# Performance work log

Measured on AMD Instinct MI355X. Metric: run time of the kernel, lower is better.

Reference implementation:

```python
import jax, jax.numpy as jnp
import numpy as np

N_NODES, N_EDGES, B, L = 20000, 320000, 64, 48
EMB, OUT, HEADS, HID = 256, 64, 4, 512
S_DIM, R_DIM = 64, 64
TIME_NUM, CAT_NUM = 48, 201


def lrelu(x, s=0.2):
    return jnp.where(x >= 0, x, s * x)


def gru_cell(x, h, Wi, Wh, bi, bh):
    # PyTorch GRUCell math
    gi = x @ Wi.T + bi
    gh = h @ Wh.T + bh
    ir, iz, ig = jnp.split(gi, 3, axis=-1)
    hr, hz, hg = jnp.split(gh, 3, axis=-1)
    r = jax.nn.sigmoid(ir + hr)
    z = jax.nn.sigmoid(iz + hz)
    n = jnp.tanh(ig + r * hg)
    return (1.0 - z) * n + z * h


def gru_seq(x, Wi, Wh, bi, bh, reverse=False):
    # x: [B,L,D] -> [B,L,H]
    xs = jnp.swapaxes(x, 0, 1)
    if reverse:
        xs = xs[::-1]
    h0 = jnp.zeros((x.shape[0], Wh.shape[1]), x.dtype)

    def step(h, xt):
        h2 = gru_cell(xt, h, Wi, Wh, bi, bh)
        return h2, h2

    _, ys = jax.lax.scan(step, h0, xs)
    if reverse:
        ys = ys[::-1]
    return jnp.swapaxes(ys, 0, 1)


def setup_inputs() -> dict:
    key = jax.random.key(0)
    ks = iter(jax.random.split(key, 64))
    f32 = jnp.float32

    def rn(shape, s=0.1):
        return (s * jax.random.normal(next(ks), shape)).astype(f32)

    inp = {
        'graph_x': jnp.arange(N_NODES),
        'edge_index': jax.random.randint(next(ks), (2, N_EDGES), 0, N_NODES),
        'edge_attr': jax.random.uniform(next(ks), (N_EDGES,), f32),
        'batch_x': jax.random.randint(next(ks), (B, L), 0, N_NODES),
        'batch_time': jax.random.randint(next(ks), (B, L), 0, TIME_NUM),
        'batch_cat': jax.random.randint(next(ks), (B, L), 0, CAT_NUM),
        'poi_time': jax.random.randint(next(ks), (N_NODES,), 0, TIME_NUM),
        'poi_cat': jax.random.randint(next(ks), (N_NODES,), 0, CAT_NUM),
        # params
        'node_emb': rn((N_NODES, EMB), 1.0),
        'W_gat': rn((EMB, HEADS * OUT), 0.05),
        'att_src': rn((HEADS, OUT), 0.05),
        'att_dst': rn((HEADS, OUT), 0.05),
        'gat_bias': rn((HEADS * OUT,)),
        'time_table': rn((TIME_NUM, EMB), 1.0),
        'cat_table': rn((CAT_NUM, EMB), 1.0),
        'W_w': rn((EMB, 3 * EMB)), 'b_w': rn((EMB,)),
        'Wi_f': rn((3 * HID, EMB), 0.05), 'Wh_f': rn((3 * HID, HID), 0.05),
        'bi_f': jnp.zeros((3 * HID,), f32), 'bh_f': jnp.zeros((3 * HID,), f32),
        'Wi_bw': rn((3 * HID, EMB), 0.05), 'Wh_bw': rn((3 * HID, HID), 0.05),
        'bi_bw': jnp.zeros((3 * HID,), f32), 'bh_bw': jnp.zeros((3 * HID,), f32),
        'Wi_u': rn((3 * HID, 2 * HID), 0.05), 'Wh_u': rn((3 * HID, HID), 0.05),
        'bi_u': jnp.zeros((3 * HID,), f32), 'bh_u': jnp.zeros((3 * HID,), f32),
        'Ws_m': rn((S_DIM, 2 * HID)), 'bs_m': rn((S_DIM,)),
        'Ws_lv': rn((S_DIM, 2 * HID)), 'bs_lv': rn((S_DIM,)),
        'Wr_m': rn((R_DIM, HID)), 'br_m': rn((R_DIM,)),
        'Wr_lv': rn((R_DIM, HID)), 'br_lv': rn((R_DIM,)),
        'Wp1_i': rn((3 * HID, R_DIM), 0.05), 'Wp1_h': rn((3 * HID, HID), 0.05),
        'bp1_i': jnp.zeros((3 * HID,), f32), 'bp1_h': jnp.zeros((3 * HID,), f32),
        'Wp2_i': rn((3 * HID, HID), 0.05), 'Wp2_h': rn((3 * HID, HID), 0.05),
        'bp2_i': jnp.zeros((3 * HID,), f32), 'bp2_h': jnp.zeros((3 * HID,), f32),
        'Wpm': rn((R_DIM, HID)), 'bpm': rn((R_DIM,)),
        'Wplv': rn((R_DIM, HID)), 'bplv': rn((R_DIM,)),
        'Wd': rn((N_NODES, S_DIM + R_DIM)), 'bd': rn((N_NODES,)),
    }
    return inp


def forward(graph_x, edge_index, edge_attr, batch_x, batch_time, batch_cat,
            poi_time, poi_cat, node_emb, W_gat, att_src, att_dst, gat_bias,
            time_table, cat_table, W_w, b_w, Wi_f, Wh_f, bi_f, bh_f,
            Wi_bw, Wh_bw, bi_bw, bh_bw, Wi_u, Wh_u, bi_u, bh_u,
            Ws_m, bs_m, Ws_lv, bs_lv, Wr_m, br_m, Wr_lv, br_lv,
            Wp1_i, Wp1_h, bp1_i, bp1_h, Wp2_i, Wp2_h, bp2_i, bp2_h,
            Wpm, bpm, Wplv, bplv, Wd, bd):
    Bn, Ln = batch_x.shape
    N = node_emb.shape[0]
    heads, C = att_src.shape

    # --- weighted GAT layer over the POI graph ---
    h = node_emb[graph_x]                                   # [N, EMB]
    xW = (h @ W_gat).reshape(N, heads, C)                   # [N, H, C]
    src, dst = edge_index[0], edge_index[1]
    e = lrelu((xW * att_src).sum(-1)[src] + (xW * att_dst).sum(-1)[dst])  # [E, H]
    emax = jax.ops.segment_max(e, dst, num_segments=N)
    a = jnp.exp(e - emax[dst])
    asum = jax.ops.segment_sum(a, dst, num_segments=N)
    att = a / (asum[dst] + 1e-16)
    msg = (att * edge_attr[:, None])[:, :, None] * xW[src]  # [E, H, C]
    p = jax.ops.segment_sum(msg, dst, num_segments=N).reshape(N, heads * C) + gat_bias

    # --- per-step feature build ---
    p_h = p[batch_x]                                        # [B, L, EMB]
    t_e = time_table[batch_time]
    c_e = cat_table[batch_cat]
    ph = jnp.concatenate([p_h, t_e, c_e], axis=2) @ W_w.T + b_w  # [B, L, EMB]

    # --- posterior encode: biGRU -> s, uniGRU -> r ---
    f_fwd = gru_seq(ph, Wi_f, Wh_f, bi_f, bh_f)
    f_bwd = gru_seq(ph, Wi_bw, Wh_bw, bi_bw, bh_bw, reverse=True)
    features = jnp.concatenate([f_fwd, f_bwd], axis=2)      # [B, L, 2H]
    Hh = Wh_f.shape[1]
    frontal = features[:, Ln - 1, :Hh]
    backward = features[:, 0, Hh:2 * Hh]
    g = jnp.concatenate([frontal, backward], axis=1)
    s_mean = lrelu(g @ Ws_m.T + bs_m)
    s_logvar = lrelu(g @ Ws_lv.T + bs_lv)

    key = jax.random.key(42)
    k1, k2, k3 = jax.random.split(key, 3)
    s_post = s_mean + jax.random.normal(k1, s_mean.shape, s_mean.dtype) * jnp.exp(0.5 * s_logvar)

    r_feat = gru_seq(features, Wi_u, Wh_u, bi_u, bh_u)      # [B, L, H]
    r_mean = r_feat @ Wr_m.T + br_m
    r_logvar = r_feat @ Wr_lv.T + br_lv
    r_post = r_mean + jax.random.normal(k2, r_mean.shape, r_mean.dtype) * jnp.exp(0.5 * r_logvar)

    # --- prior: 2-layer GRUCell unroll fed with shifted r_post ---
    Rd = r_post.shape[2]
    r_in = jnp.concatenate([jnp.zeros((Bn, 1, Rd), r_post.dtype), r_post[:, :-1]], axis=1)
    r_in_t = jnp.swapaxes(r_in, 0, 1)                       # [L, B, R]
    eps = jax.random.normal(k3, (Ln, Bn, Rd), r_post.dtype)

    def pstep(carry, xe):
        h1, h2 = carry
        rt, ep = xe
        h1 = gru_cell(rt, h1, Wp1_i, Wp1_h, bp1_i, bp1_h)
        h2 = gru_cell(h1, h2, Wp2_i, Wp2_h, bp2_i, bp2_h)
        mt = h2 @ Wpm.T + bpm
        lvt = h2 @ Wplv.T + bplv
        rp = mt + ep * jnp.exp(0.5 * lvt)
        return (h1, h2), (mt, lvt, rp)

    h10 = jnp.zeros((Bn, Hh), r_post.dtype)
    h20 = jnp.zeros((Bn, Hh), r_post.dtype)
    _, (ms, lvs, rps) = jax.lax.scan(pstep, (h10, h20), (r_in_t, eps))
    r_mean_prior = jnp.swapaxes(ms, 0, 1)
    r_logvar_prior = jnp.swapaxes(lvs, 0, 1)
    r_prior = jnp.swapaxes(rps, 0, 1)

    # --- decode ---
    s_expand = jnp.broadcast_to(s_post[:, None, :], (Bn, Ln, s_post.shape[1]))
    zf = jnp.concatenate([r_post, s_expand], axis=2)
    recon_x = zf @ Wd.T + bd                                # [B, L, node_num]
    return (s_mean, s_logvar, s_post, r_mean, r_logvar, r_post,
            r_mean_prior, r_logvar_prior, r_prior, recon_x)


def reference(graph_x, edge_index, edge_attr, batch_x, batch_time, batch_cat,
              poi_time, poi_cat, node_emb, W_gat, att_src, att_dst, gat_bias,
              time_table, cat_table, W_w, b_w, Wi_f, Wh_f, bi_f, bh_f,
              Wi_bw, Wh_bw, bi_bw, bh_bw, Wi_u, Wh_u, bi_u, bh_u,
              Ws_m, bs_m, Ws_lv, bs_lv, Wr_m, br_m, Wr_lv, br_lv,
              Wp1_i, Wp1_h, bp1_i, bp1_h, Wp2_i, Wp2_h, bp2_i, bp2_h,
              Wpm, bpm, Wplv, bplv, Wd, bd):
    return forward(graph_x, edge_index, edge_attr, batch_x, batch_time, batch_cat,
                   poi_time, poi_cat, node_emb, W_gat, att_src, att_dst, gat_bias,
                   time_table, cat_table, W_w, b_w, Wi_f, Wh_f, bi_f, bh_f,
                   Wi_bw, Wh_bw, bi_bw, bh_bw, Wi_u, Wh_u, bi_u, bh_u,
                   Ws_m, bs_m, Ws_lv, bs_lv, Wr_m, br_m, Wr_lv, br_lv,
                   Wp1_i, Wp1_h, bp1_i, bp1_h, Wp2_i, Wp2_h, bp2_i, bp2_h,
                   Wpm, bpm, Wplv, bplv, Wd, bd)
```

## Files before the change

kernel.cpp:

```cpp
#include <hip/hip_runtime.h>
#include <stdint.h>
#include <stddef.h>

#define DEV __device__ __forceinline__

typedef float f32x4 __attribute__((ext_vector_type(4)));
typedef short bf16x8 __attribute__((ext_vector_type(8)));

__host__ __device__ inline void tf2x32(uint32_t k0, uint32_t k1,
                                       uint32_t x0, uint32_t x1,
                                       uint32_t* o0, uint32_t* o1) {
  uint32_t ks2 = k0 ^ k1 ^ 0x1BD11BDAu;
  uint32_t ks[3] = {k0, k1, ks2};
  x0 += k0; x1 += k1;
  const uint32_t R[8] = {13u,15u,26u,6u,17u,29u,16u,24u};
  for (int r = 0; r < 5; ++r) {
    const uint32_t* rot = (r & 1) ? (R + 4) : R;
    for (int i = 0; i < 4; ++i) {
      x0 += x1;
      uint32_t d = rot[i];
      x1 = (x1 << d) | (x1 >> (32u - d));
      x1 ^= x0;
    }
    x0 += ks[(r + 1) % 3];
    x1 += ks[(r + 2) % 3] + (uint32_t)(r + 1);
  }
  *o0 = x0; *o1 = x1;
}

DEV float erfinv_approx(float x) {
  float w = -logf((1.0f - x) * (1.0f + x));
  float p;
  if (w < 5.0f) {
    w = w - 2.5f;
    p = 2.81022636e-08f;
    p = fmaf(p, w, 3.43273939e-07f);
    p = fmaf(p, w, -3.5233877e-06f);
    p = fmaf(p, w, -4.39150654e-06f);
    p = fmaf(p, w, 0.00021858087f);
    p = fmaf(p, w, -0.00125372503f);
    p = fmaf(p, w, -0.00417768164f);
    p = fmaf(p, w, 0.246640727f);
    p = fmaf(p, w, 1.50140941f);
  } else {
    w = sqrtf(w) - 3.0f;
    p = -0.000200214257f;
    p = fmaf(p, w, 0.000100950558f);
    p = fmaf(p, w, 0.00134934322f);
    p = fmaf(p, w, -0.00367342844f);
    p = fmaf(p, w, 0.00573950773f);
    p = fmaf(p, w, -0.0076224613f);
    p = fmaf(p, w, 0.00943887047f);
    p = fmaf(p, w, 1.00167406f);
    p = fmaf(p, w, 2.83297682f);
  }
  return p * x;
}

DEV float normal_part(uint32_t ka, uint32_t kb, uint32_t idx) {
  uint32_t b1, b2;
  tf2x32(ka, kb, 0u, idx, &b1, &b2);
  uint32_t bits = b1 ^ b2;
  float f = __uint_as_float((bits >> 9) | 0x3f800000u) - 1.0f;
  const float lo = -0.99999994f;
  float u = f * 2.0f + lo;
  u = fmaxf(lo, u);
  return 1.41421356f * erfinv_approx(u);
}

DEV float lrelu(float x) { return x >= 0.f ? x : 0.2f * x; }
DEV float sigm(float x) { return 1.0f / (1.0f + expf(-x)); }

DEV float gru_out(float ir, float iz, float ig, float hr, float hz, float hg, float hprev) {
  float r = sigm(ir + hr);
  float z = sigm(iz + hz);
  float n = tanhf(ig + r * hg);
  return (1.0f - z) * n + z * hprev;
}

DEV float dot4f(float4 a, float4 b, float acc) {
  return fmaf(a.x, b.x, fmaf(a.y, b.y, fmaf(a.z, b.z, fmaf(a.w, b.w, acc))));
}

template <int K4>
DEV void dot2(const float* __restrict__ h, const float* __restrict__ w0,
              const float* __restrict__ w1, float& a0, float& a1) {
  const float4* h4 = (const float4*)h;
  const float4* p0 = (const float4*)w0;
  const float4* p1 = (const float4*)w1;
  #pragma unroll 4
  for (int k = 0; k < K4; ++k) {
    float4 hv = h4[k];
    float4 v0 = p0[k], v1 = p1[k];
    a0 = dot4f(hv, v0, a0);
    a1 = dot4f(hv, v1, a1);
  }
}

template <int K4>
DEV void dotT3p(const float* __restrict__ hp, int b,
                const float* __restrict__ w0, const float* __restrict__ w1,
                const float* __restrict__ w2, float& a0, float& a1, float& a2) {
  const float4* __restrict__ w04 = (const float4*)w0;
  const float4* __restrict__ w14 = (const float4*)w1;
  const float4* __restrict__ w24 = (const float4*)w2;
  const float4* __restrict__ h4 = (const float4*)hp;
  #pragma unroll
  for (int k4 = 0; k4 < K4; ++k4) {
    float4 hv = h4[k4 * 64 + b];
    a0 = dot4f(w04[k4], hv, a0);
    a1 = dot4f(w14[k4], hv, a1);
    a2 = dot4f(w24[k4], hv, a2);
  }
}

template <int K4>
DEV void dotT3_lds(const float* __restrict__ hl, int b,
                   const float* __restrict__ w0, const float* __restrict__ w1,
                   const float* __restrict__ w2, float& a0, float& a1, float& a2) {
  const float4* __restrict__ h4 = (const float4*)hl;
  const float4* __restrict__ w04 = (const float4*)w0;
  const float4* __restrict__ w14 = (const float4*)w1;
  const float4* __restrict__ w24 = (const float4*)w2;
  #pragma unroll 8
  for (int k4 = 0; k4 < K4; ++k4) {
    float4 hv = h4[k4 * 64 + b];
    a0 = dot4f(w04[k4], hv, a0);
    a1 = dot4f(w14[k4], hv, a1);
    a2 = dot4f(w24[k4], hv, a2);
  }
}

template <int N16>
DEV void stage_lds(float* __restrict__ dst, const float* __restrict__ src) {
  const float4* __restrict__ s4 = (const float4*)src;
  float4* __restrict__ d4 = (float4*)dst;
  int tid = threadIdx.x;
  constexpr int CH = (N16 < 16) ? N16 : 16;
  #pragma unroll
  for (int r = 0; r < N16; r += CH) {
    float4 v[CH];
    #pragma unroll
    for (int u = 0; u < CH; ++u) v[u] = s4[(size_t)(r + u) * 256 + tid];
    #pragma unroll
    for (int u = 0; u < CH; ++u) d4[(size_t)(r + u) * 256 + tid] = v[u];
  }
}

DEV size_t pk(int k, int b) { return (size_t)(k >> 2) * 256 + b * 4 + (k & 3); }

DEV void coh_store_i(int* p, int v) {
  asm volatile("global_store_dword %0, %1, off sc0 sc1" :: "v"(p), "v"(v) : "memory");
}
DEV void coh_store_f(float* p, float v) {
  asm volatile("global_store_dword %0, %1, off sc0 sc1" :: "v"(p), "v"(v) : "memory");
}
DEV void coh_store_f4(float* p, f32x4 v) {
  asm volatile("global_store_dwordx4 %0, %1, off sc0 sc1" :: "v"(p), "v"(v) : "memory");
}
DEV int coh_load_i(const int* p) {
  int v;
  asm volatile("global_load_dword %0, %1, off sc0 sc1\n\ts_waitcnt vmcnt(0)"
               : "=v"(v) : "v"(p) : "memory");
  return v;
}

#define FSTRIDE 32

DEV void flag_barrier(int* __restrict__ flags, int nblk, int myidx, int gen) {
  asm volatile("s_waitcnt vmcnt(0)" ::: "memory");
  __syncthreads();
  if (threadIdx.x == 0) coh_store_i(flags + (size_t)myidx * FSTRIDE, gen);
  if ((int)threadIdx.x < nblk) {
    int spins = 0;
    while (coh_load_i(flags + (size_t)threadIdx.x * FSTRIDE) < gen) {
      __builtin_amdgcn_s_sleep(4);
      if (++spins > (1 << 21)) break;
    }
  }
  __syncthreads();
}

DEV void wait_group(const int* __restrict__ flags, int nblk, int thr) {
  if ((int)threadIdx.x < nblk) {
    int spins = 0;
    while (coh_load_i(flags + (size_t)threadIdx.x * FSTRIDE) < thr) {
      __builtin_amdgcn_s_sleep(4);
      if (++spins > (1 << 21)) break;
    }
  }
  __syncthreads();
}

DEV void store_packed_tile4(float* dst_t, const float (*smem)[64], int j0) {
  if (threadIdx.x < 64) {
    int bb = threadIdx.x;
    f32x4 v;
    v.x = smem[0][bb];
    v.y = smem[1][bb];
    v.z = smem[2][bb];
    v.w = smem[3][bb];
    coh_store_f4(dst_t + (size_t)(j0 >> 2) * 256 + bb * 4, v);
  }
}

#define GBM 128
#define GBN 128
#define GBK 16

__global__ __launch_bounds__(256) void gemm_nt(
    const float* __restrict__ A, const float* __restrict__ Bt,
    const float* __restrict__ bias, float* __restrict__ C,
    int M, int N, int K, const int* __restrict__ gatherA, int trGI) {
  __shared__ float As[GBK][GBM + 4];
  __shared__ float Bs[GBK][GBN + 4];
  const int bm = blockIdx.y * GBM;
  const int bn = blockIdx.x * GBN;
  const int tid = threadIdx.x;
  const int tx = tid & 15;
  const int ty = tid >> 4;
  float acc[8][8];
  #pragma unroll
  for (int i = 0; i < 8; ++i)
    #pragma unroll
    for (int j = 0; j < 8; ++j) acc[i][j] = 0.f;

  for (int k0 = 0; k0 < K; k0 += GBK) {
    #pragma unroll
    for (int s = 0; s < 2; ++s) {
      int f = tid + s * 256;
      int r = f >> 2, kq = f & 3;
      int row = bm + r;
      float4 v = make_float4(0.f, 0.f, 0.f, 0.f);
      if (row < M) {
        int ar = gatherA ? gatherA[row] : row;
        v = *(const float4*)&A[(size_t)ar * K + k0 + kq * 4];
      }
      As[kq * 4 + 0][r] = v.x;
      As[kq * 4 + 1][r] = v.y;
      As[kq * 4 + 2][r] = v.z;
      As[kq * 4 + 3][r] = v.w;
    }
    #pragma unroll
    for (int s = 0; s < 2; ++s) {
      int f = tid + s * 256;
      int r = f >> 2, kq = f & 3;
      int col = bn + r;
      float4 v = make_float4(0.f, 0.f, 0.f, 0.f);
      if (col < N) v = *(const float4*)&Bt[(size_t)col * K + k0 + kq * 4];
      Bs[kq * 4 + 0][r] = v.x;
      Bs[kq * 4 + 1][r] = v.y;
      Bs[kq * 4 + 2][r] = v.z;
      Bs[kq * 4 + 3][r] = v.w;
    }
    __syncthreads();
    #pragma unroll
    for (int kk = 0; kk < GBK; ++kk) {
      float4 a0 = *(const float4*)&As[kk][ty * 4];
      float4 a1 = *(const float4*)&As[kk][64 + ty * 4];
      float4 b0 = *(const float4*)&Bs[kk][tx * 4];
      float4 b1 = *(const float4*)&Bs[kk][64 + tx * 4];
      float av[8] = {a0.x, a0.y, a0.z, a0.w, a1.x, a1.y, a1.z, a1.w};
      float bv[8] = {b0.x, b0.y, b0.z, b0.w, b1.x, b1.y, b1.z, b1.w};
      #pragma unroll
      for (int i = 0; i < 8; ++i)
        #pragma unroll
        for (int j = 0; j < 8; ++j)
          acc[i][j] = fmaf(av[i], bv[j], acc[i][j]);
    }
    __syncthreads();
  }
  #pragma unroll
  for (int i = 0; i < 8; ++i) {
    int row = bm + ((i < 4) ? (ty * 4 + i) : (64 + ty * 4 + i - 4));
    if (row >= M) continue;
    if (trGI) {
      #pragma unroll
      for (int j = 0; j < 8; ++j) {
        int col = bn + ((j < 4) ? (tx * 4 + j) : (64 + tx * 4 + j - 4));
        if (col >= N) continue;
        float v = acc[i][j] + (bias ? bias[col] : 0.f);
        int bb = row / 48, tt = row - bb * 48;
        C[((size_t)tt * N + col) * 64 + bb] = v;
      }
    } else {
      #pragma unroll
      for (int g = 0; g < 2; ++g) {
        int col0 = bn + g * 64 + tx * 4;
        if (col0 + 3 >= N) continue;
        float4 v;
        v.x = acc[i][g * 4 + 0] + (bias ? bias[col0 + 0] : 0.f);
        v.y = acc[i][g * 4 + 1] + (bias ? bias[col0 + 1] : 0.f);
        v.z = acc[i][g * 4 + 2] + (bias ? bias[col0 + 2] : 0.f);
        v.w = acc[i][g * 4 + 3] + (bias ? bias[col0 + 3] : 0.f);
        *(float4*)&C[(size_t)row * N + col0] = v;
      }
    }
  }
}

__global__ void k_f32_to_bf16(const float* __restrict__ src,
                              unsigned short* __restrict__ dst, int n) {
  int i = blockIdx.x * 256 + threadIdx.x;
  if (i >= n) return;
  uint32_t u = __float_as_uint(src[i]);
  uint32_t r = (u + 0x7fffu + ((u >> 16) & 1u)) >> 16;
  dst[i] = (unsigned short)r;
}

__global__ __launch_bounds__(256) void gemm_bf16_mfma(
    const unsigned short* __restrict__ A16, const unsigned short* __restrict__ B16,
    const float* __restrict__ bias, float* __restrict__ C,
    int M, int N, int K, int trGI) {
  int bm = blockIdx.x * 128;
  int bn = blockIdx.y * 128;
  int wave = threadIdx.x >> 6;
  int lane = threadIdx.x & 63;
  int wm = (wave & 1) * 64;
  int wn = (wave >> 1) * 64;
  int l15 = lane & 15;
  int kg = lane >> 4;
  f32x4 acc[4][4];
  #pragma unroll
  for (int mi = 0; mi < 4; ++mi)
    #pragma unroll
    for (int ni = 0; ni < 4; ++ni)
      acc[mi][ni] = (f32x4){0.f, 0.f, 0.f, 0.f};

  for (int kk = 0; kk < K; kk += 32) {
    bf16x8 afrag[4], bfrag[4];
    #pragma unroll
    for (int mi = 0; mi < 4; ++mi) {
      int row = bm + wm + mi * 16 + l15;
      afrag[mi] = *(const bf16x8*)&A16[(size_t)row * K + kk + kg * 8];
    }
    #pragma unroll
    for (int ni = 0; ni < 4; ++ni) {
      int col = bn + wn + ni * 16 + l15;
      if (col >= N) col = N - 1;
      bfrag[ni] = *(const bf16x8*)&B16[(size_t)col * K + kk + kg * 8];
    }
    #pragma unroll
    for (int mi = 0; mi < 4; ++mi)
      #pragma unroll
      for (int ni = 0; ni < 4; ++ni)
        acc[mi][ni] = __builtin_amdgcn_mfma_f32_16x16x32_bf16(
            afrag[mi], bfrag[ni], acc[mi][ni], 0, 0, 0);
  }
  #pragma unroll
  for (int mi = 0; mi < 4; ++mi) {
    #pragma unroll
    for (int ni = 0; ni < 4; ++ni) {
      int col = bn + wn + ni * 16 + l15;
      if (col >= N) continue;
      int rowb = bm + wm + mi * 16 + kg * 4;
      float bv = bias ? bias[col] : 0.f;
      if (trGI) {
        #pragma unroll
        for (int r = 0; r < 4; ++r) {
          int row = rowb + r;
          int bb = row / 48, tt = row - bb * 48;
          C[((size_t)tt * N + col) * 64 + bb] = acc[mi][ni][r] + bv;
        }
      } else {
        #pragma unroll
        for (int r = 0; r < 4; ++r)
          C[(size_t)(rowb + r) * N + col] = acc[mi][ni][r] + bv;
      }
    }
  }
}

__global__ void k_transpose(const float* __restrict__ W, float* __restrict__ Wt,
                            int rows, int cols) {
  int idx = blockIdx.x * 256 + threadIdx.x;
  if (idx >= rows * cols) return;
  int r = idx / cols, c = idx % cols;
  Wt[(size_t)c * rows + r] = W[idx];
}

__global__ void k_count_deg(const int* __restrict__ dst, int* __restrict__ deg, int nE) {
  int e = blockIdx.x * 256 + threadIdx.x;
  if (e < nE) atomicAdd(&deg[dst[e]], 1);
}

__global__ __launch_bounds__(1024) void k_scan(const int* __restrict__ deg,
                                               int* __restrict__ off,
                                               int* __restrict__ cursor, int n) {
  __shared__ int tmp[1024];
  __shared__ int carry_s;
  if (threadIdx.x == 0) carry_s = 0;
  __syncthreads();
  for (int base = 0; base < n; base += 1024) {
    int i = base + (int)threadIdx.x;
    int v = (i < n) ? deg[i] : 0;
    tmp[threadIdx.x] = v;
    __syncthreads();
    for (int s = 1; s < 1024; s <<= 1) {
      int t = (threadIdx.x >= (unsigned)s) ? tmp[threadIdx.x - s] : 0;
      __syncthreads();
      tmp[threadIdx.x] += t;
      __syncthreads();
    }
    int incl = tmp[threadIdx.x];
    int base_c = carry_s;
    int excl = incl - v;
    if (i < n) { off[i] = base_c + excl; cursor[i] = base_c + excl; }
    __syncthreads();
    if (threadIdx.x == 1023) carry_s = base_c + incl;
    __syncthreads();
  }
  if (threadIdx.x == 0) off[n] = carry_s;
}

__global__ void k_scatter(const int* __restrict__ dst, int* __restrict__ cursor,
                          int* __restrict__ csr, int nE) {
  int e = blockIdx.x * 256 + threadIdx.x;
  if (e < nE) {
    int pos = atomicAdd(&cursor[dst[e]], 1);
    csr[pos] = e;
  }
}

__global__ void k_alpha(const float* __restrict__ xW, const float* __restrict__ att_src,
                        const float* __restrict__ att_dst, float* __restrict__ as_,
                        float* __restrict__ ad_) {
  int i = blockIdx.x * 256 + threadIdx.x;
  if (i >= 80000) return;
  int n = i >> 2, h = i & 3;
  const float* xr = xW + (size_t)n * 256 + h * 64;
  const float* s = att_src + h * 64;
  const float* d = att_dst + h * 64;
  float a = 0.f, b = 0.f;
  dot2<16>(xr, s, d, a, b);
  as_[i] = a;
  ad_[i] = b;
}

__global__ __launch_bounds__(256) void k_gat_node(
    const float* __restrict__ xW, const float* __restrict__ as_,
    const float* __restrict__ ad_, const int* __restrict__ off,
    const int* __restrict__ csr, const int* __restrict__ esrc,
    const float* __restrict__ eattr, const float* __restrict__ gat_bias,
    float* __restrict__ p) {
  int n = blockIdx.x;
  int h = threadIdx.x >> 6;
  int c = threadIdx.x & 63;
  int s0 = off[n], s1 = off[n + 1];
  float adn = ad_[n * 4 + h];
  float m = -3.0e38f;
  for (int idx = s0; idx < s1; ++idx) {
    int e = csr[idx];
    int s = esrc[e];
    float ev = lrelu(as_[s * 4 + h] + adn);
    m = fmaxf(m, ev);
  }
  float sum = 0.f;
  for (int idx = s0; idx < s1; ++idx) {
    int e = csr[idx];
    int s = esrc[e];
    float ev = lrelu(as_[s * 4 + h] + adn);
    sum += expf(ev - m);
  }
  float acc = 0.f;
  for (int idx = s0; idx < s1; ++idx) {
    int e = csr[idx];
    int s = esrc[e];
    float ev = lrelu(as_[s * 4 + h] + adn);
    float w = expf(ev - m) / (sum + 1e-16f) * eattr[e];
    acc = fmaf(w, xW[(size_t)s * 256 + h * 64 + c], acc);
  }
  p[(size_t)n * 256 + h * 64 + c] = acc + gat_bias[h * 64 + c];
}

__global__ void k_build_X(const float* __restrict__ p, const float* __restrict__ tt,
                          const float* __restrict__ ct, const int* __restrict__ bx,
                          const int* __restrict__ btm, const int* __restrict__ bct,
                          float* __restrict__ X) {
  int idx = blockIdx.x * 256 + threadIdx.x;
  if (idx >= 3072 * 768) return;
  int rl = idx / 768, c = idx % 768;
  float v;
  if (c < 256) v = p[(size_t)bx[rl] * 256 + c];
  else if (c < 512) v = tt[(size_t)btm[rl] * 256 + (c - 256)];
  else v = ct[(size_t)bct[rl] * 256 + (c - 512)];
  X[idx] = v;
}

__global__ __launch_bounds__(256, 1) void k_gru_bidir_fused(
    const float* __restrict__ giT_f, const float* __restrict__ giT_b,
    const float* __restrict__ Wh_f, const float* __restrict__ bh_f,
    const float* __restrict__ Wh_b, const float* __restrict__ bh_b,
    float* __restrict__ features, float* __restrict__ hTb,
    int* __restrict__ flags) {
  __shared__ float lds_h[32768];
  __shared__ float smem[4][64];
  int w = threadIdx.x >> 6;
  int b = threadIdx.x & 63;
  int slot = blockIdx.x * 4 + w;
  int dir = slot >> 9;
  int j = slot & 511;
  int j0 = (blockIdx.x * 4) & 511;
  int gbid = blockIdx.x & 127;
  int* gflags = flags + (size_t)dir * 128 * FSTRIDE;
  const float* Wh = dir ? Wh_b : Wh_f;
  const float* bh = dir ? bh_b : bh_f;
  const float* gi = dir ? giT_b : giT_f;
  const float* w0 = Wh + (size_t)j * 512;
  const float* w1 = Wh + (size_t)(512 + j) * 512;
  const float* w2 = Wh + (size_t)(1024 + j) * 512;
  float bhr = bh[j], bhz = bh[512 + j], bhg = bh[1024 + j];
  float* hD = hTb + (size_t)dir * 48 * 32768;
  for (int s = 0; s < 48; ++s) {
    int t = dir ? (47 - s) : s;
    const float* gir = gi + (size_t)t * 98304;
    float giv0 = gir[j * 64 + b];
    float giv1 = gir[(512 + j) * 64 + b];
    float giv2 = gir[(1024 + j) * 64 + b];
    float hr = bhr, hz = bhz, hg = bhg, hprev = 0.f;
    if (s > 0) {
      int tp = dir ? (t + 1) : (t - 1);
      stage_lds<32>(lds_h, hD + (size_t)tp * 32768);
      __syncthreads();
      dotT3_lds<128>(lds_h, b, w0, w1, w2, hr, hz, hg);
      hprev = lds_h[pk(j, b)];
    }
    float hnew = gru_out(giv0, giv1, giv2, hr, hz, hg, hprev);
    smem[w][b] = hnew;
    features[((size_t)(b * 48 + t)) * 1024 + dir * 512 + j] = hnew;
    __syncthreads();
    store_packed_tile4(hD + (size_t)t * 32768, smem, j0);
    flag_barrier(gflags, 128, gbid, s + 1);
  }
}

__global__ __launch_bounds__(256, 1) void k_gru_u_fused(
    const float* __restrict__ giT, const float* __restrict__ Wh,
    const float* __restrict__ bh, float* __restrict__ r_feat,
    float* __restrict__ hU, int* __restrict__ flags) {
  __shared__ float lds_h[32768];
  __shared__ float smem[4][64];
  int w = threadIdx.x >> 6;
  int b = threadIdx.x & 63;
  int j = blockIdx.x * 4 + w;
  int j0 = blockIdx.x * 4;
  const float* w0 = Wh + (size_t)j * 512;
  const float* w1 = Wh + (size_t)(512 + j) * 512;
  const float* w2 = Wh + (size_t)(1024 + j) * 512;
  float bhr = bh[j], bhz = bh[512 + j], bhg = bh[1024 + j];
  for (int s = 0; s < 48; ++s) {
    const float* gir = giT + (size_t)s * 98304;
    float giv0 = gir[j * 64 + b];
    float giv1 = gir[(512 + j) * 64 + b];
    float giv2 = gir[(1024 + j) * 64 + b];
    float hr = bhr, hz = bhz, hg = bhg, hprev = 0.f;
    if (s > 0) {
      stage_lds<32>(lds_h, hU + (size_t)(s - 1) * 32768);
      __syncthreads();
      dotT3_lds<128>(lds_h, b, w0, w1, w2, hr, hz, hg);
      hprev = lds_h[pk(j, b)];
    }
    float hnew = gru_out(giv0, giv1, giv2, hr, hz, hg, hprev);
    smem[w][b] = hnew;
    r_feat[((size_t)(b * 48 + s)) * 512 + j] = hnew;
    __syncthreads();
    store_packed_tile4(hU + (size_t)s * 32768, smem, j0);
    flag_barrier(flags, 128, blockIdx.x, s + 1);
  }
}

__global__ __launch_bounds__(256, 1) void k_prior_fused(
    const float* __restrict__ r_post,
    const float* __restrict__ Wp1_i, const float* __restrict__ Wp1_h,
    const float* __restrict__ bp1_i, const float* __restrict__ bp1_h,
    const float* __restrict__ Wp2_i, const float* __restrict__ Wp2_h,
    const float* __restrict__ bp2_i, const float* __restrict__ bp2_h,
    float* __restrict__ h1S, float* __restrict__ h2S,
    float* __restrict__ rT, int* __restrict__ flags) {
  __shared__ float lds_h[32768];
  __shared__ float smem[4][64];
  int w = threadIdx.x >> 6;
  int b = threadIdx.x & 63;
  int cell = blockIdx.x >> 7;
  int gbid = blockIdx.x & 127;
  int slot = blockIdx.x * 4 + w;
  int j = slot & 511;
  int j0 = (blockIdx.x * 4) & 511;
  int* flagsA = flags;
  int* flagsB = flags + (size_t)128 * FSTRIDE;

  if (cell == 0) {
    int tid = gbid * 256 + threadIdx.x;
    for (int x = tid; x < 48 * 64 * 64; x += 32768) {
      int b0 = x & 63;
      int i0 = (x >> 6) & 63;
      int t0 = x >> 12;
      coh_store_f(rT + (size_t)t0 * 4096 + pk(i0, b0),
                  r_post[((size_t)(b0 * 48 + t0)) * 64 + i0]);
    }
    flag_barrier(flagsA, 128, gbid, 1);

    const float* wi0 = Wp1_i + (size_t)j * 64;
    const float* wi1 = Wp1_i + (size_t)(512 + j) * 64;
    const float* wi2 = Wp1_i + (size_t)(1024 + j) * 64;
    const float* wh0 = Wp1_h + (size_t)j * 512;
    const float* wh1 = Wp1_h + (size_t)(512 + j) * 512;
    const float* wh2 = Wp1_h + (size_t)(1024 + j) * 512;
    float bir = bp1_i[j], biz = bp1_i[512 + j], big = bp1_i[1024 + j];
    float bhr = bp1_h[j], bhz = bp1_h[512 + j], bhg = bp1_h[1024 + j];
    for (int k = 0; k < 48; ++k) {
      float ir = bir, iz = biz, ig = big;
      float hr = bhr, hz = bhz, hg = bhg, hprev = 0.f;
      if (k > 0) {
        stage_lds<32>(lds_h, h1S + (size_t)(k - 1) * 32768);
        dotT3p<16>(rT + (size_t)(k - 1) * 4096, b, wi0, wi1, wi2, ir, iz, ig);
        __syncthreads();
        dotT3_lds<128>(lds_h, b, wh0, wh1, wh2, hr, hz, hg);
        hprev = lds_h[pk(j, b)];
      }
      smem[w][b] = gru_out(ir, iz, ig, hr, hz, hg, hprev);
      __syncthreads();
      store_packed_tile4(h1S + (size_t)k * 32768, smem, j0);
      flag_barrier(flagsA, 128, gbid, k + 2);
    }
  } else {
    const float* wi0 = Wp2_i + (size_t)j * 512;
    const float* wi1 = Wp2_i + (size_t)(512 + j) * 512;
    const float* wi2 = Wp2_i + (size_t)(1024 + j) * 512;
    const float* wh0 = Wp2_h + (size_t)j * 512;
    const float* wh1 = Wp2_h + (size_t)(512 + j) * 512;
    const float* wh2 = Wp2_h + (size_t)(1024 + j) * 512;
    float bir = bp2_i[j], biz = bp2_i[512 + j], big = bp2_i[1024 + j];
    float bhr = bp2_h[j], bhz = bp2_h[512 + j], bhg = bp2_h[1024 + j];
    for (int t = 0; t < 48; ++t) {
      wait_group(flagsA, 128, t + 2);
      stage_lds<32>(lds_h, h1S + (size_t)t * 32768);
      __syncthreads();
      float ir = bir, iz = biz, ig = big;
      dotT3_lds<128>(lds_h, b, wi0, wi1, wi2, ir, iz, ig);
      float hr = bhr, hz = bhz, hg = bhg, hprev = 0.f;
      if (t > 0) {
        __syncthreads();
        stage_lds<32>(lds_h, h2S + (size_t)(t - 1) * 32768);
        __syncthreads();
        dotT3_lds<128>(lds_h, b, wh0, wh1, wh2, hr, hz, hg);
        hprev = lds_h[pk(j, b)];
      }
      smem[w][b] = gru_out(ir, iz, ig, hr, hz, hg, hprev);
      __syncthreads();
      store_packed_tile4(h2S + (size_t)t * 32768, smem, j0);
      flag_barrier(flagsB, 128, gbid, t + 1);
    }
  }
}

__global__ void k_s_head(const float* __restrict__ features,
                         const float* __restrict__ Ws_m, const float* __restrict__ bs_m,
                         const float* __restrict__ Ws_lv, const float* __restrict__ bs_lv,
                         float* __restrict__ out, uint32_t ka, uint32_t kb) {
  int idx = blockIdx.x * 256 + threadIdx.x;
  if (idx >= 4096) return;
  int i = idx & 63, b = idx >> 6;
  const float* fr = features + ((size_t)(b * 48 + 47)) * 1024;
  const float* bk = features + ((size_t)(b * 48 + 0)) * 1024 + 512;
  const float* wm = Ws_m + (size_t)i * 1024;
  const float* wl = Ws_lv + (size_t)i * 1024;
  float m = 0.f, lv = 0.f;
  dot2<128>(fr, wm, wl, m, lv);
  dot2<128>(bk, wm + 512, wl + 512, m, lv);
  m = lrelu(m + bs_m[i]);
  lv = lrelu(lv + bs_lv[i]);
  float nz = normal_part(ka, kb, (uint32_t)idx);
  out[idx] = m;
  out[4096 + idx] = lv;
  out[8192 + idx] = m + nz * expf(0.5f * lv);
}

__global__ void k_r_head(const float* __restrict__ r_feat,
                         const float* __restrict__ Wr_m, const float* __restrict__ br_m,
                         const float* __restrict__ Wr_lv, const float* __restrict__ br_lv,
                         float* __restrict__ out, uint32_t ka, uint32_t kb) {
  int idx = blockIdx.x * 256 + threadIdx.x;
  if (idx >= 196608) return;
  int i = idx & 63;
  int bt = idx >> 6;
  const float* f = r_feat + (size_t)bt * 512;
  float m = 0.f, lv = 0.f;
  dot2<128>(f, Wr_m + (size_t)i * 512, Wr_lv + (size_t)i * 512, m, lv);
  m += br_m[i];
  lv += br_lv[i];
  float nz = normal_part(ka, kb, (uint32_t)idx);
  out[12288 + idx] = m;
  out[208896 + idx] = lv;
  out[405504 + idx] = m + nz * expf(0.5f * lv);
}

__global__ void k_prior_out(const float* __restrict__ h2S,
                            const float* __restrict__ Wpm, const float* __restrict__ bpm,
                            const float* __restrict__ Wplv, const float* __restrict__ bplv,
                            float* __restrict__ out, uint32_t ka, uint32_t kb) {
  int idx = blockIdx.x * 256 + threadIdx.x;
  if (idx >= 196608) return;
  int i = idx & 63;
  int bt = idx >> 6;
  int b = bt & 63;
  int t = bt >> 6;
  const float4* h4 = (const float4*)(h2S + (size_t)t * 32768);
  const float4* wm4 = (const float4*)(Wpm + (size_t)i * 512);
  const float4* wl4 = (const float4*)(Wplv + (size_t)i * 512);
  float m = 0.f, lv = 0.f;
  #pragma unroll 8
  for (int k4 = 0; k4 < 128; ++k4) {
    float4 hv = h4[k4 * 64 + b];
    m = dot4f(wm4[k4], hv, m);
    lv = dot4f(wl4[k4], hv, lv);
  }
  m += bpm[i];
  lv += bplv[i];
  float ep = normal_part(ka, kb, (uint32_t)idx);
  float rp = m + ep * expf(0.5f * lv);
  size_t o = ((size_t)b * 48 + t) * 64 + i;
  out[602112 + o] = m;
  out[798720 + o] = lv;
  out[995328 + o] = rp;
}

__global__ void k_build_zf(const float* __restrict__ out, float* __restrict__ zf) {
  int idx = blockIdx.x * 256 + threadIdx.x;
  if (idx >= 3072 * 128) return;
  int row = idx >> 7, c = idx & 127;
  float v;
  if (c < 64) v = out[405504 + row * 64 + c];
  else v = out[8192 + (row / 48) * 64 + (c - 64)];
  zf[idx] = v;
}

extern "C" void kernel_launch(void* const* d_in, const int* in_sizes, int n_in,
                              void* d_out, int out_size, void* d_ws, size_t ws_size,
                              hipStream_t stream) {
  const int* graph_x = (const int*)d_in[0];
  const int* edge_index = (const int*)d_in[1];
  const float* edge_attr = (const float*)d_in[2];
  const int* batch_x = (const int*)d_in[3];
  const int* batch_time = (const int*)d_in[4];
  const int* batch_cat = (const int*)d_in[5];
  const float* node_emb = (const float*)d_in[8];
  const float* W_gat = (const float*)d_in[9];
  const float* att_src = (const float*)d_in[10];
  const float* att_dst = (const float*)d_in[11];
  const float* gat_bias = (const float*)d_in[12];
  const float* time_table = (const float*)d_in[13];
  const float* cat_table = (const float*)d_in[14];
  const float* W_w = (const float*)d_in[15];
  const float* b_w = (const float*)d_in[16];
  const float* Wi_f = (const float*)d_in[17];
  const float* Wh_f = (const float*)d_in[18];
  const float* bi_f = (const float*)d_in[19];
  const float* bh_f = (const float*)d_in[20];
  const float* Wi_bw = (const float*)d_in[21];
  const float* Wh_bw = (const float*)d_in[22];
  const float* bi_bw = (const float*)d_in[23];
  const float* bh_bw = (const float*)d_in[24];
  const float* Wi_u = (const float*)d_in[25];
  const float* Wh_u = (const float*)d_in[26];
  const float* bi_u = (const float*)d_in[27];
  const float* bh_u = (const float*)d_in[28];
  const float* Ws_m = (const float*)d_in[29];
  const float* bs_m = (const float*)d_in[30];
  const float* Ws_lv = (const float*)d_in[31];
  const float* bs_lv = (const float*)d_in[32];
  const float* Wr_m = (const float*)d_in[33];
  const float* br_m = (const float*)d_in[34];
  const float* Wr_lv = (const float*)d_in[35];
  const float* br_lv = (const float*)d_in[36];
  const float* Wp1_i = (const float*)d_in[37];
  const float* Wp1_h = (const float*)d_in[38];
  const float* bp1_i = (const float*)d_in[39];
  const float* bp1_h = (const float*)d_in[40];
  const float* Wp2_i = (const float*)d_in[41];
  const float* Wp2_h = (const float*)d_in[42];
  const float* bp2_i = (const float*)d_in[43];
  const float* bp2_h = (const float*)d_in[44];
  const float* Wpm = (const float*)d_in[45];
  const float* bpm = (const float*)d_in[46];
  const float* Wplv = (const float*)d_in[47];
  const float* bplv = (const float*)d_in[48];
  const float* Wd = (const float*)d_in[49];
  const float* bd = (const float*)d_in[50];
  float* out = (float*)d_out;

  uint32_t k1a, k1b, k2a, k2b, k3a, k3b;
  tf2x32(0u, 42u, 0u, 0u, &k1a, &k1b);
  tf2x32(0u, 42u, 0u, 1u, &k2a, &k2b);
  tf2x32(0u, 42u, 0u, 2u, &k3a, &k3b);

  float* ws = (float*)d_ws;
  size_t o = 0;
  auto alloc = [&](size_t n) { float* q = ws + o; o += n; return q; };
  float* R1 = alloc(5120000);
  float* R2 = alloc(5120000);
  float* R3 = alloc(4718592);
  float* R4 = alloc(786432);
  float* as_ = alloc(80000);
  float* ad_ = alloc(80000);
  float* Wgt = alloc(65536);
  int* deg = (int*)alloc(20000);
  int* off = (int*)alloc(20001);
  int* cursor = (int*)alloc(20000);
  int* csr = (int*)alloc(320000);
  float* rT = alloc(196608);
  int* flags = (int*)alloc(32768);

  float* xW = R1;
  float* features = R1;
  float* r_feat = R1 + 3145728;
  float* p = R2;
  float* giT_b = R2;
  float* hU = R2;
  float* X = R3;
  float* giT_f = R3;
  float* giT_u = R3;
  float* h1S = R3;
  float* h2S = R3 + 1572864;
  float* ph = R4;
  float* zf = R4;
  unsigned short* ph16 = (unsigned short*)R1;
  unsigned short* Wif16 = (unsigned short*)(R1 + 1000000);
  unsigned short* Wib16 = (unsigned short*)(R1 + 1500000);
  unsigned short* Wiu16 = (unsigned short*)R2;
  unsigned short* feat16 = (unsigned short*)(R2 + 1000000);
  unsigned short* Wd16 = (unsigned short*)R2;
  unsigned short* zf16 = (unsigned short*)(R4 + 458752);
  float* hTb = out + 1191936;

  const int* esrc = edge_index;
  const int* edst = edge_index + 320000;

  dim3 B(256);

  (void)hipMemsetAsync(deg, 0, 20000 * sizeof(int), stream);
  (void)hipMemsetAsync(flags, 0, 32768 * sizeof(int), stream);

  k_transpose<<<dim3(256), B, 0, stream>>>(W_gat, Wgt, 256, 256);
  k_count_deg<<<dim3(1250), B, 0, stream>>>(edst, deg, 320000);
  k_scan<<<dim3(1), dim3(1024), 0, stream>>>(deg, off, cursor, 20000);
  k_scatter<<<dim3(1250), B, 0, stream>>>(edst, cursor, csr, 320000);
  gemm_nt<<<dim3(2, 157), B, 0, stream>>>(node_emb, Wgt, nullptr, xW,
                                          20000, 256, 256, graph_x, 0);
  k_alpha<<<dim3(313), B, 0, stream>>>(xW, att_src, att_dst, as_, ad_);
  k_gat_node<<<dim3(20000), B, 0, stream>>>(xW, as_, ad_, off, csr, esrc,
                                            edge_attr, gat_bias, p);

  k_build_X<<<dim3(9216), B, 0, stream>>>(p, time_table, cat_table, batch_x,
                                          batch_time, batch_cat, X);
  gemm_nt<<<dim3(2, 24), B, 0, stream>>>(X, W_w, b_w, ph, 3072, 256, 768,
                                         nullptr, 0);

  k_f32_to_bf16<<<dim3(3072), B, 0, stream>>>(ph, ph16, 3072 * 256);
  k_f32_to_bf16<<<dim3(1536), B, 0, stream>>>(Wi_f, Wif16, 1536 * 256);
  k_f32_to_bf16<<<dim3(1536), B, 0, stream>>>(Wi_bw, Wib16, 1536 * 256);
  gemm_bf16_mfma<<<dim3(24, 12), B, 0, stream>>>(ph16, Wif16, bi_f, giT_f,
                                                 3072, 1536, 256, 1);
  gemm_bf16_mfma<<<dim3(24, 12), B, 0, stream>>>(ph16, Wib16, bi_bw, giT_b,
                                                 3072, 1536, 256, 1);
  k_gru_bidir_fused<<<dim3(256), B, 0, stream>>>(
      giT_f, giT_b, Wh_f, bh_f, Wh_bw, bh_bw, features, hTb, flags);

  k_s_head<<<dim3(16), B, 0, stream>>>(features, Ws_m, bs_m, Ws_lv, bs_lv,
                                       out, k1a, k1b);

  k_f32_to_bf16<<<dim3(12288), B, 0, stream>>>(features, feat16, 3072 * 1024);
  k_f32_to_bf16<<<dim3(6144), B, 0, stream>>>(Wi_u, Wiu16, 1536 * 1024);
  gemm_bf16_mfma<<<dim3(24, 12), B, 0, stream>>>(feat16, Wiu16, bi_u, giT_u,
                                                 3072, 1536, 1024, 1);
  k_gru_u_fused<<<dim3(128), B, 0, stream>>>(giT_u, Wh_u, bh_u, r_feat,
                                             hU, flags + 256 * FSTRIDE);

  k_f32_to_bf16<<<dim3(10000), B, 0, stream>>>(Wd, Wd16, 20000 * 128);

  k_r_head<<<dim3(768), B, 0, stream>>>(r_feat, Wr_m, br_m, Wr_lv, br_lv,
                                        out, k2a, k2b);

  k_prior_fused<<<dim3(256), B, 0, stream>>>(
      out + 405504, Wp1_i, Wp1_h, bp1_i, bp1_h, Wp2_i, Wp2_h, bp2_i, bp2_h,
      h1S, h2S, rT, flags + 384 * FSTRIDE);
  k_prior_out<<<dim3(768), B, 0, stream>>>(h2S, Wpm, bpm, Wplv, bplv,
                                           out, k3a, k3b);

  k_build_zf<<<dim3(1536), B, 0, stream>>>(out, zf);
  k_f32_to_bf16<<<dim3(1536), B, 0, stream>>>(zf, zf16, 3072 * 128);
  gemm_bf16_mfma<<<dim3(24, 157), B, 0, stream>>>(zf16, Wd16, bd,
                                                  out + 1191936, 3072, 20000, 128, 0);
}
```

Measured before the change: 4.537 ms.

## Fuse GRU-u, r-head and two-layer prior GRU into one pipelined persistent kernel

Replaces the separate GRU-u recurrence, r-head and prior GRU kernels with a single persistent kernel of 192 blocks split into three roles. The u-GRU role computes the r-head per timestep and feeds r_post to the prior cell 1, which feeds prior cell 2 through per-timestep flag barriers. The three recurrences therefore run as a wavefront instead of one after another. Each block now handles 8 hidden units instead of 4, so each flag barrier spans 64 blocks, which lowers barrier cost but doubles the serial work per block. The h1S/h2S scratch moves into the output buffer region so it does not collide with the live buffers.

```diff
diff --git a/kernel.cpp b/kernel.cpp
--- a/kernel.cpp
+++ b/kernel.cpp
@@ -201,6 +201,19 @@
     v.z = smem[2][bb];
     v.w = smem[3][bb];
     coh_store_f4(dst_t + (size_t)(j0 >> 2) * 256 + bb * 4, v);
+  }
+}
+
+DEV void store_packed_tile8(float* dst_t, const float (*smem)[64], int j0) {
+  if (threadIdx.x < 128) {
+    int q = threadIdx.x >> 6;
+    int bb = threadIdx.x & 63;
+    f32x4 v;
+    v.x = smem[q * 4 + 0][bb];
+    v.y = smem[q * 4 + 1][bb];
+    v.z = smem[q * 4 + 2][bb];
+    v.w = smem[q * 4 + 3][bb];
+    coh_store_f4(dst_t + (size_t)((j0 >> 2) + q) * 256 + bb * 4, v);
   }
 }
 
@@ -534,122 +547,204 @@
   }
 }
 
-__global__ __launch_bounds__(256, 1) void k_gru_u_fused(
-    const float* __restrict__ giT, const float* __restrict__ Wh,
-    const float* __restrict__ bh, float* __restrict__ r_feat,
-    float* __restrict__ hU, int* __restrict__ flags) {
-  __shared__ float lds_h[32768];
-  __shared__ float smem[4][64];
-  int w = threadIdx.x >> 6;
-  int b = threadIdx.x & 63;
-  int j = blockIdx.x * 4 + w;
-  int j0 = blockIdx.x * 4;
-  const float* w0 = Wh + (size_t)j * 512;
-  const float* w1 = Wh + (size_t)(512 + j) * 512;
-  const float* w2 = Wh + (size_t)(1024 + j) * 512;
-  float bhr = bh[j], bhz = bh[512 + j], bhg = bh[1024 + j];
-  for (int s = 0; s < 48; ++s) {
-    const float* gir = giT + (size_t)s * 98304;
-    float giv0 = gir[j * 64 + b];
-    float giv1 = gir[(512 + j) * 64 + b];
-    float giv2 = gir[(1024 + j) * 64 + b];
-    float hr = bhr, hz = bhz, hg = bhg, hprev = 0.f;
-    if (s > 0) {
-      stage_lds<32>(lds_h, hU + (size_t)(s - 1) * 32768);
-      __syncthreads();
-      dotT3_lds<128>(lds_h, b, w0, w1, w2, hr, hz, hg);
-      hprev = lds_h[pk(j, b)];
-    }
-    float hnew = gru_out(giv0, giv1, giv2, hr, hz, hg, hprev);
-    smem[w][b] = hnew;
-    r_feat[((size_t)(b * 48 + s)) * 512 + j] = hnew;
-    __syncthreads();
-    store_packed_tile4(hU + (size_t)s * 32768, smem, j0);
-    flag_barrier(flags, 128, blockIdx.x, s + 1);
-  }
-}
-
-__global__ __launch_bounds__(256, 1) void k_prior_fused(
-    const float* __restrict__ r_post,
+__global__ __launch_bounds__(256, 1) void k_upr(
+    const float* __restrict__ giT_u, const float* __restrict__ Wh_u,
+    const float* __restrict__ bh_u,
+    const float* __restrict__ Wr_m, const float* __restrict__ br_m,
+    const float* __restrict__ Wr_lv, const float* __restrict__ br_lv,
     const float* __restrict__ Wp1_i, const float* __restrict__ Wp1_h,
     const float* __restrict__ bp1_i, const float* __restrict__ bp1_h,
     const float* __restrict__ Wp2_i, const float* __restrict__ Wp2_h,
     const float* __restrict__ bp2_i, const float* __restrict__ bp2_h,
-    float* __restrict__ h1S, float* __restrict__ h2S,
-    float* __restrict__ rT, int* __restrict__ flags) {
+    float* __restrict__ hU, float* __restrict__ h1S, float* __restrict__ h2S,
+    float* __restrict__ rfT, float* __restrict__ rT,
+    float* __restrict__ out, uint32_t k2a, uint32_t k2b,
+    int* __restrict__ flags) {
   __shared__ float lds_h[32768];
-  __shared__ float smem[4][64];
+  __shared__ float smem[8][64];
+  __shared__ float smemR[4][64][2];
+  int role = blockIdx.x >> 6;
+  int g = blockIdx.x & 63;
   int w = threadIdx.x >> 6;
   int b = threadIdx.x & 63;
-  int cell = blockIdx.x >> 7;
-  int gbid = blockIdx.x & 127;
-  int slot = blockIdx.x * 4 + w;
-  int j = slot & 511;
-  int j0 = (blockIdx.x * 4) & 511;
-  int* flagsA = flags;
-  int* flagsB = flags + (size_t)128 * FSTRIDE;
-
-  if (cell == 0) {
-    int tid = gbid * 256 + threadIdx.x;
-    for (int x = tid; x < 48 * 64 * 64; x += 32768) {
-      int b0 = x & 63;
-      int i0 = (x >> 6) & 63;
-      int t0 = x >> 12;
-      coh_store_f(rT + (size_t)t0 * 4096 + pk(i0, b0),
-                  r_post[((size_t)(b0 * 48 + t0)) * 64 + i0]);
-    }
-    flag_barrier(flagsA, 128, gbid, 1);
-
-    const float* wi0 = Wp1_i + (size_t)j * 64;
-    const float* wi1 = Wp1_i + (size_t)(512 + j) * 64;
-    const float* wi2 = Wp1_i + (size_t)(1024 + j) * 64;
-    const float* wh0 = Wp1_h + (size_t)j * 512;
-    const float* wh1 = Wp1_h + (size_t)(512 + j) * 512;
-    const float* wh2 = Wp1_h + (size_t)(1024 + j) * 512;
-    float bir = bp1_i[j], biz = bp1_i[512 + j], big = bp1_i[1024 + j];
-    float bhr = bp1_h[j], bhz = bp1_h[512 + j], bhg = bp1_h[1024 + j];
+  int j0 = g * 8;
+  int* uflags = flags;
+  int* c1flags = flags + (size_t)64 * FSTRIDE;
+  int* c2flags = flags + (size_t)128 * FSTRIDE;
+
+  if (role == 0) {
+    for (int s = 0; s < 48; ++s) {
+      if (s > 0) stage_lds<32>(lds_h, hU + (size_t)(s - 1) * 32768);
+      if (s > 0) {
+        int i = threadIdx.x & 63;
+        int wv = threadIdx.x >> 6;
+        const float* rrow = rfT + (size_t)(s - 1) * 32768;
+        const float* wmrow = Wr_m + (size_t)i * 512;
+        const float* wlrow = Wr_lv + (size_t)i * 512;
+        float pm = 0.f, plv = 0.f;
+        #pragma unroll 8
+        for (int k = wv * 128; k < wv * 128 + 128; ++k) {
+          float hvv = rrow[k * 64 + g];
+          pm = fmaf(hvv, wmrow[k], pm);
+          plv = fmaf(hvv, wlrow[k], plv);
+        }
+        smemR[wv][i][0] = pm;
+        smemR[wv][i][1] = plv;
+      }
+      __syncthreads();
+      if (s > 0 && threadIdx.x < 64) {
+        int i = threadIdx.x;
+        float m = smemR[0][i][0] + smemR[1][i][0] + smemR[2][i][0] +
+                  smemR[3][i][0] + br_m[i];
+        float lv = smemR[0][i][1] + smemR[1][i][1] + smemR[2][i][1] +
+                   smemR[3][i][1] + br_lv[i];
+        uint32_t idx = ((uint32_t)(g * 48 + (s - 1)) << 6) | (uint32_t)i;
+        float nz = normal_part(k2a, k2b, idx);
+        float rp = m + nz * expf(0.5f * lv);
+        out[12288 + idx] = m;
+        out[208896 + idx] = lv;
+        out[405504 + idx] = rp;
+        coh_store_f(rT + (size_t)(s - 1) * 4096 + pk(i, g), rp);
+      }
+      float hn[2];
+      #pragma unroll
+      for (int p = 0; p < 2; ++p) {
+        int j = j0 + p * 4 + w;
+        const float* gir = giT_u + (size_t)s * 98304;
+        float g0 = gir[j * 64 + b];
+        float g1 = gir[(512 + j) * 64 + b];
+        float g2 = gir[(1024 + j) * 64 + b];
+        float hr = bh_u[j], hz = bh_u[512 + j], hg = bh_u[1024 + j];
+        float hp = 0.f;
+        if (s > 0) {
+          dotT3_lds<128>(lds_h, b, Wh_u + (size_t)j * 512,
+                         Wh_u + (size_t)(512 + j) * 512,
+                         Wh_u + (size_t)(1024 + j) * 512, hr, hz, hg);
+          hp = lds_h[pk(j, b)];
+        }
+        hn[p] = gru_out(g0, g1, g2, hr, hz, hg, hp);
+      }
+      smem[w][b] = hn[0];
+      smem[4 + w][b] = hn[1];
+      __syncthreads();
+      store_packed_tile8(hU + (size_t)s * 32768, smem, j0);
+      if (threadIdx.x < 128) {
+        int t = threadIdx.x;
+        int jj = t >> 4;
+        int b4 = (t & 15) * 4;
+        f32x4 v;
+        v.x = smem[jj][b4 + 0];
+        v.y = smem[jj][b4 + 1];
+        v.z = smem[jj][b4 + 2];
+        v.w = smem[jj][b4 + 3];
+        coh_store_f4(rfT + (size_t)s * 32768 + (size_t)(j0 + jj) * 64 + b4, v);
+      }
+      flag_barrier(uflags, 64, g, s + 1);
+    }
+    {
+      int i = threadIdx.x & 63;
+      int wv = threadIdx.x >> 6;
+      const float* rrow = rfT + (size_t)47 * 32768;
+      const float* wmrow = Wr_m + (size_t)i * 512;
+      const float* wlrow = Wr_lv + (size_t)i * 512;
+      float pm = 0.f, plv = 0.f;
+      #pragma unroll 8
+      for (int k = wv * 128; k < wv * 128 + 128; ++k) {
+        float hvv = rrow[k * 64 + g];
+        pm = fmaf(hvv, wmrow[k], pm);
+        plv = fmaf(hvv, wlrow[k], plv);
+      }
+      smemR[wv][i][0] = pm;
+      smemR[wv][i][1] = plv;
+      __syncthreads();
+      if (threadIdx.x < 64) {
+        int i2 = threadIdx.x;
+        float m = smemR[0][i2][0] + smemR[1][i2][0] + smemR[2][i2][0] +
+                  smemR[3][i2][0] + br_m[i2];
+        float lv = smemR[0][i2][1] + smemR[1][i2][1] + smemR[2][i2][1] +
+                   smemR[3][i2][1] + br_lv[i2];
+        uint32_t idx = ((uint32_t)(g * 48 + 47) << 6) | (uint32_t)i2;
+        float nz = normal_part(k2a, k2b, idx);
+        float rp = m + nz * expf(0.5f * lv);
+        out[12288 + idx] = m;
+        out[208896 + idx] = lv;
+        out[405504 + idx] = rp;
+      }
+    }
+  } else if (role == 1) {
     for (int k = 0; k < 48; ++k) {
-      float ir = bir, iz = biz, ig = big;
-      float hr = bhr, hz = bhz, hg = bhg, hprev = 0.f;
       if (k > 0) {
+        wait_group(uflags, 64, k + 1);
         stage_lds<32>(lds_h, h1S + (size_t)(k - 1) * 32768);
-        dotT3p<16>(rT + (size_t)(k - 1) * 4096, b, wi0, wi1, wi2, ir, iz, ig);
-        __syncthreads();
-        dotT3_lds<128>(lds_h, b, wh0, wh1, wh2, hr, hz, hg);
-        hprev = lds_h[pk(j, b)];
-      }
-      smem[w][b] = gru_out(ir, iz, ig, hr, hz, hg, hprev);
-      __syncthreads();
-      store_packed_tile4(h1S + (size_t)k * 32768, smem, j0);
-      flag_barrier(flagsA, 128, gbid, k + 2);
+      }
+      __syncthreads();
+      float hn[2];
+      #pragma unroll
+      for (int p = 0; p < 2; ++p) {
+        int j = j0 + p * 4 + w;
+        float ir = bp1_i[j], iz = bp1_i[512 + j], ig = bp1_i[1024 + j];
+        float hr = bp1_h[j], hz = bp1_h[512 + j], hg = bp1_h[1024 + j];
+        float hp = 0.f;
+        if (k > 0) {
+          dotT3p<16>(rT + (size_t)(k - 1) * 4096, b,
+                     Wp1_i + (size_t)j * 64, Wp1_i + (size_t)(512 + j) * 64,
+                     Wp1_i + (size_t)(1024 + j) * 64, ir, iz, ig);
+          dotT3_lds<128>(lds_h, b, Wp1_h + (size_t)j * 512,
+                         Wp1_h + (size_t)(512 + j) * 512,
+                         Wp1_h + (size_t)(1024 + j) * 512, hr, hz, hg);
+          hp = lds_h[pk(j, b)];
+        }
+        hn[p] = gru_out(ir, iz, ig, hr, hz, hg, hp);
+      }
+      smem[w][b] = hn[0];
+      smem[4 + w][b] = hn[1];
+      __syncthreads();
+      store_packed_tile8(h1S + (size_t)k * 32768, smem, j0);
+      flag_barrier(c1flags, 64, g, k + 1);
     }
   } else {
-    const float* wi0 = Wp2_i + (size_t)j * 512;
-    const float* wi1 = Wp2_i + (size_t)(512 + j) * 512;
-    const float* wi2 = Wp2_i + (size_t)(1024 + j) * 512;
-    const float* wh0 = Wp2_h + (size_t)j * 512;
-    const float* wh1 = Wp2_h + (size_t)(512 + j) * 512;
-    const float* wh2 = Wp2_h + (size_t)(1024 + j) * 512;
-    float bir = bp2_i[j], biz = bp2_i[512 + j], big = bp2_i[1024 + j];
-    float bhr = bp2_h[j], bhz = bp2_h[512 + j], bhg = bp2_h[1024 + j];
     for (int t = 0; t < 48; ++t) {
-      wait_group(flagsA, 128, t + 2);
+      wait_group(c1flags, 64, t + 1);
       stage_lds<32>(lds_h, h1S + (size_t)t * 32768);
       __syncthreads();
-      float ir = bir, iz = biz, ig = big;
-      dotT3_lds<128>(lds_h, b, wi0, wi1, wi2, ir, iz, ig);
-      float hr = bhr, hz = bhz, hg = bhg, hprev = 0.f;
+      float iv0[2], iv1[2], iv2[2];
+      #pragma unroll
+      for (int p = 0; p < 2; ++p) {
+        int j = j0 + p * 4 + w;
+        float a0 = bp2_i[j], a1 = bp2_i[512 + j], a2 = bp2_i[1024 + j];
+        dotT3_lds<128>(lds_h, b, Wp2_i + (size_t)j * 512,
+                       Wp2_i + (size_t)(512 + j) * 512,
+                       Wp2_i + (size_t)(1024 + j) * 512, a0, a1, a2);
+        iv0[p] = a0; iv1[p] = a1; iv2[p] = a2;
+      }
+      __syncthreads();
+      float hn[2];
       if (t > 0) {
-        __syncthreads();
         stage_lds<32>(lds_h, h2S + (size_t)(t - 1) * 32768);
         __syncthreads();
-        dotT3_lds<128>(lds_h, b, wh0, wh1, wh2, hr, hz, hg);
-        hprev = lds_h[pk(j, b)];
-      }
-      smem[w][b] = gru_out(ir, iz, ig, hr, hz, hg, hprev);
-      __syncthreads();
-      store_packed_tile4(h2S + (size_t)t * 32768, smem, j0);
-      flag_barrier(flagsB, 128, gbid, t + 1);
+        #pragma unroll
+        for (int p = 0; p < 2; ++p) {
+          int j = j0 + p * 4 + w;
+          float hr = bp2_h[j], hz = bp2_h[512 + j], hg = bp2_h[1024 + j];
+          dotT3_lds<128>(lds_h, b, Wp2_h + (size_t)j * 512,
+                         Wp2_h + (size_t)(512 + j) * 512,
+                         Wp2_h + (size_t)(1024 + j) * 512, hr, hz, hg);
+          float hp = lds_h[pk(j, b)];
+          hn[p] = gru_out(iv0[p], iv1[p], iv2[p], hr, hz, hg, hp);
+        }
+      } else {
+        #pragma unroll
+        for (int p = 0; p < 2; ++p) {
+          int j = j0 + p * 4 + w;
+          hn[p] = gru_out(iv0[p], iv1[p], iv2[p], bp2_h[j], bp2_h[512 + j],
+                          bp2_h[1024 + j], 0.f);
+        }
+      }
+      smem[w][b] = hn[0];
+      smem[4 + w][b] = hn[1];
+      __syncthreads();
+      store_packed_tile8(h2S + (size_t)t * 32768, smem, j0);
+      flag_barrier(c2flags, 64, g, t + 1);
     }
   }
 }
@@ -674,25 +769,6 @@
   out[idx] = m;
   out[4096 + idx] = lv;
   out[8192 + idx] = m + nz * expf(0.5f * lv);
-}
-
-__global__ void k_r_head(const float* __restrict__ r_feat,
-                         const float* __restrict__ Wr_m, const float* __restrict__ br_m,
-                         const float* __restrict__ Wr_lv, const float* __restrict__ br_lv,
-                         float* __restrict__ out, uint32_t ka, uint32_t kb) {
-  int idx = blockIdx.x * 256 + threadIdx.x;
-  if (idx >= 196608) return;
-  int i = idx & 63;
-  int bt = idx >> 6;
-  const float* f = r_feat + (size_t)bt * 512;
-  float m = 0.f, lv = 0.f;
-  dot2<128>(f, Wr_m + (size_t)i * 512, Wr_lv + (size_t)i * 512, m, lv);
-  m += br_m[i];
-  lv += br_lv[i];
-  float nz = normal_part(ka, kb, (uint32_t)idx);
-  out[12288 + idx] = m;
-  out[208896 + idx] = lv;
-  out[405504 + idx] = m + nz * expf(0.5f * lv);
 }
 
 __global__ void k_prior_out(const float* __restrict__ h2S,
@@ -813,15 +889,13 @@
 
   float* xW = R1;
   float* features = R1;
-  float* r_feat = R1 + 3145728;
+  float* rfT = R1 + 3145728;
   float* p = R2;
   float* giT_b = R2;
   float* hU = R2;
   float* X = R3;
   float* giT_f = R3;
   float* giT_u = R3;
-  float* h1S = R3;
-  float* h2S = R3 + 1572864;
   float* ph = R4;
   float* zf = R4;
   unsigned short* ph16 = (unsigned short*)R1;
@@ -832,6 +906,8 @@
   unsigned short* Wd16 = (unsigned short*)R2;
   unsigned short* zf16 = (unsigned short*)(R4 + 458752);
   float* hTb = out + 1191936;
+  float* h1S = out + 1191936 + 3145728;
+  float* h2S = h1S + 1572864;
 
   const int* esrc = edge_index;
   const int* edst = edge_index + 320000;
@@ -873,17 +949,14 @@
   k_f32_to_bf16<<<dim3(6144), B, 0, stream>>>(Wi_u, Wiu16, 1536 * 1024);
   gemm_bf16_mfma<<<dim3(24, 12), B, 0, stream>>>(feat16, Wiu16, bi_u, giT_u,
                                                  3072, 1536, 1024, 1);
-  k_gru_u_fused<<<dim3(128), B, 0, stream>>>(giT_u, Wh_u, bh_u, r_feat,
-                                             hU, flags + 256 * FSTRIDE);
+
+  k_upr<<<dim3(192), B, 0, stream>>>(
+      giT_u, Wh_u, bh_u, Wr_m, br_m, Wr_lv, br_lv,
+      Wp1_i, Wp1_h, bp1_i, bp1_h, Wp2_i, Wp2_h, bp2_i, bp2_h,
+      hU, h1S, h2S, rfT, rT, out, k2a, k2b, flags + 256 * FSTRIDE);
 
   k_f32_to_bf16<<<dim3(10000), B, 0, stream>>>(Wd, Wd16, 20000 * 128);
 
-  k_r_head<<<dim3(768), B, 0, stream>>>(r_feat, Wr_m, br_m, Wr_lv, br_lv,
-                                        out, k2a, k2b);
-
-  k_prior_fused<<<dim3(256), B, 0, stream>>>(
-      out + 405504, Wp1_i, Wp1_h, bp1_i, bp1_h, Wp2_i, Wp2_h, bp2_i, bp2_h,
-      h1S, h2S, rT, flags + 384 * FSTRIDE);
   k_prior_out<<<dim3(768), B, 0, stream>>>(h2S, Wpm, bpm, Wplv, bplv,
                                            out, k3a, k3b);
 
```

Result: slower. 5.228 ms (+15.2%).
